# Kernel optimization log

Measured on AMD Instinct MI355X. Metric: run time of the kernel, lower is better.

Reference implementation:

```python
import jax, jax.numpy as jnp
import numpy as np
from jax import lax

B, T, V = 32, 2048, 32  # batch, num observations (frames), state vocabulary


def setup_inputs() -> dict:
    key = jax.random.key(0)
    k1, k2, k3, k4, k5 = jax.random.split(key, 5)
    inputs = jax.random.normal(k1, (B, T, V, V), dtype=jnp.float32)
    targets = jax.random.randint(k2, (B, T + 1), 0, V)  # state sequence z_0..z_T
    transition = 0.1 * jax.random.normal(k3, (V, V), dtype=jnp.float32)
    initial = 0.1 * jax.random.normal(k4, (V,), dtype=jnp.float32)
    final = 0.1 * jax.random.normal(k5, (V,), dtype=jnp.float32)
    return {"inputs": inputs, "transition": transition, "initial": initial,
            "final": final, "targets": targets}


def _log_prob(inputs, transition, initial, final, targets):
    # inputs: [B,T,V,V] arc scores score[b,t,i,j] for transition i->j at step t
    # Lattice semantics (compose(obs_fst, seq_fst)): a path is z_0..z_T with
    #   weight = initial[z_0] + sum_t (score[t, z_t, z_{t+1}] + A[z_t, z_{t+1}]) + final[z_T]
    b, t = inputs.shape[0], inputs.shape[1]
    v = transition.shape[0]

    # ---- denominator: forward algorithm (log-sum-exp DP over the lattice) ----
    scores_t = jnp.transpose(inputs, (1, 0, 2, 3))  # [T,B,V,V]
    alpha0 = jnp.broadcast_to(initial[None, :], (b, v))  # [B,V]

    def step(alpha, s_t):
        # alpha: [B,V] over previous state i; s_t: [B,V,V]
        m = alpha[:, :, None] + s_t + transition[None, :, :]  # [B,V,V]
        return jax.nn.logsumexp(m, axis=1), None

    alphaT, _ = lax.scan(step, alpha0, scores_t)
    denom = jax.nn.logsumexp(alphaT + final[None, :], axis=-1)  # [B]

    # ---- numerator: score of the ground-truth path ----
    y_prev = targets[:, :-1]  # [B,T]
    y_next = targets[:, 1:]   # [B,T]
    flat = inputs.reshape(b, t, v * v)
    emit = jnp.take_along_axis(flat, (y_prev * v + y_next)[..., None], axis=2)[..., 0]  # [B,T]
    trans = transition[y_prev, y_next]  # [B,T]
    num = (initial[targets[:, 0]]
           + jnp.sum(emit + trans, axis=1)
           + final[targets[:, -1]])  # [B]

    return num - denom  # log p(targets | inputs), per sequence: [B]


def reference(inputs, transition, initial, final, targets):
    return _log_prob(inputs, transition, initial, final, targets)
```

## Files before the change

### kernel.cpp

```cpp
#include <hip/hip_runtime.h>
#include <hip/hip_bf16.h>
#include <cmath>

#define Bz 32
#define Tz 2048
#define Vz 32
#define Cz 64
#define Lz 32
#define WPB 4

typedef short short8 __attribute__((ext_vector_type(8)));
typedef float f32x16 __attribute__((ext_vector_type(16)));
typedef float f32x4  __attribute__((ext_vector_type(4)));

static __device__ __forceinline__ unsigned short f2bf(float x) {
    unsigned u = __builtin_bit_cast(unsigned, x);
    u += 0x7FFFu + ((u >> 16) & 1u);
    return (unsigned short)(u >> 16);
}

static __device__ __forceinline__ void gl_lds16(const float* g, float* l) {
    __builtin_amdgcn_global_load_lds(
        (const __attribute__((address_space(1))) void*)g,
        (__attribute__((address_space(3))) void*)l, 16, 0, 0);
}

__global__ void __launch_bounds__(256) crf_chunks(
    const float* __restrict__ inputs, const float* __restrict__ trans,
    const int* __restrict__ targets, float* __restrict__ Pout,
    float* __restrict__ numpart)
{
    __shared__ __align__(16) float trans_lds[1024];
    __shared__ __align__(16) float sbuf[WPB][3 * 1024];
    __shared__ __align__(16) unsigned short elds[WPB][32 * 40];
    __shared__ __align__(16) float cbuf[WPB][32];

    const int tid  = threadIdx.x;
    const int lane = tid & 63;
    const int wid  = tid >> 6;
    const int gid  = __builtin_amdgcn_readfirstlane(blockIdx.x * WPB + wid);
    const int b    = gid >> 6;
    const int c    = gid & (Cz - 1);

    const int h = lane >> 5;
    const int j = lane & 31;
    const int kbase = 8 * h;

    float tr[16];
#pragma unroll
    for (int e = 0; e < 8; ++e) {
        tr[e]     = trans[(kbase + e) * Vz + j];
        tr[8 + e] = trans[(16 + kbase + e) * Vz + j];
    }

    ((float4*)trans_lds)[tid] = ((const float4*)trans)[tid];
    __syncthreads();

    const float* src = inputs + ((size_t)b * Tz + (size_t)c * Lz) * (Vz * Vz);
    const int*   tgb = targets + b * (Tz + 1) + c * Lz;
    int tgv = (lane < Lz + 1) ? tgb[lane] : 0;

    float* sw = sbuf[wid];
    {
        const float* g0 = src + lane * 4;
#pragma unroll
        for (int q = 0; q < 4; ++q) gl_lds16(g0 + q * 256, sw + q * 256);
        const float* g1 = src + 1024 + lane * 4;
#pragma unroll
        for (int q = 0; q < 4; ++q) gl_lds16(g1 + q * 256, sw + 1024 + q * 256);
    }

    f32x16 p;
    float cj = 0.f;
    float epart = 0.f;
    float ckr[16];
#pragma unroll
    for (int e = 0; e < 16; ++e) ckr[e] = 0.f;

    for (int t = 0; t < Lz; ++t) {
        if (t + 2 < Lz) {
            const float* g = src + (t + 2) * 1024 + lane * 4;
            float* dst = sw + ((t + 2) % 3) * 1024;
#pragma unroll
            for (int q = 0; q < 4; ++q) gl_lds16(g + q * 256, dst + q * 256);
        }
        const int rem = Lz - 1 - t;
        if (rem >= 2)      { asm volatile("s_waitcnt vmcnt(8)" ::: "memory"); }
        else if (rem == 1) { asm volatile("s_waitcnt vmcnt(4)" ::: "memory"); }
        else               { asm volatile("s_waitcnt vmcnt(0)" ::: "memory"); }
        __builtin_amdgcn_sched_barrier(0);

        const float* sb = sw + (t % 3) * 1024;

        {
            int yp = __shfl(tgv, t, 64);
            int yn = __shfl(tgv, t + 1, 64);
            int eidx = yp * Vz + yn;
            epart += sb[eidx] + trans_lds[eidx];
        }

        float m[16];
#pragma unroll
        for (int e = 0; e < 8; ++e) {
            m[e]     = sb[(kbase + e) * Vz + j]      + tr[e]     + ckr[e];
            m[8 + e] = sb[(16 + kbase + e) * Vz + j] + tr[8 + e] + ckr[8 + e];
        }
        float d = m[0];
#pragma unroll
        for (int e = 1; e < 16; ++e) d = fmaxf(d, m[e]);
        d = fmaxf(d, __shfl_xor(d, 32, 64));

        short8 B1, B2;
#pragma unroll
        for (int e = 0; e < 8; ++e) {
            B1[e] = (short)f2bf(__expf(m[e] - d));
            B2[e] = (short)f2bf(__expf(m[8 + e] - d));
        }

        short8 A1, A2;
        if (t == 0) {
#pragma unroll
            for (int e = 0; e < 8; ++e) {
                A1[e] = (short)((kbase + e == j) ? 0x3F80 : 0);
                A2[e] = (short)((16 + kbase + e == j) ? 0x3F80 : 0);
            }
        } else {
            const unsigned short* ew = elds[wid] + j * 40;
            A1 = *(const short8*)(ew + kbase);
            A2 = *(const short8*)(ew + 16 + kbase);
        }

        f32x16 z = {};
        p = __builtin_amdgcn_mfma_f32_32x32x16_bf16(A1, B1, z, 0, 0, 0);
        p = __builtin_amdgcn_mfma_f32_32x32x16_bf16(A2, B2, p, 0, 0, 0);

        float mj = p[0];
#pragma unroll
        for (int r = 1; r < 16; ++r) mj = fmaxf(mj, p[r]);
        mj = fmaxf(mj, __shfl_xor(mj, 32, 64));
        float inv = 1.0f / mj;
#pragma unroll
        for (int r = 0; r < 16; ++r) p[r] *= inv;
        cj = d + __logf(mj);

        unsigned short* ew = elds[wid];
#pragma unroll
        for (int r = 0; r < 16; ++r) {
            const int row = (r & 3) + 8 * (r >> 2) + 4 * h;
            ew[row * 40 + j] = f2bf(p[r]);
        }
        if (lane < 32) cbuf[wid][j] = cj;
        {
            const float* cb = cbuf[wid];
            f32x4 c0 = *(const f32x4*)(cb + kbase);
            f32x4 c1 = *(const f32x4*)(cb + kbase + 4);
            f32x4 c2 = *(const f32x4*)(cb + 16 + kbase);
            f32x4 c3 = *(const f32x4*)(cb + 16 + kbase + 4);
#pragma unroll
            for (int v = 0; v < 4; ++v) {
                ckr[v] = c0[v]; ckr[4 + v] = c1[v];
                ckr[8 + v] = c2[v]; ckr[12 + v] = c3[v];
            }
        }
    }

    float* Pc = Pout + (size_t)gid * 1024;
#pragma unroll
    for (int r = 0; r < 16; ++r) {
        const int row = (r & 3) + 8 * (r >> 2) + 4 * h;
        Pc[row * Vz + j] = cj + __logf(p[r]);
    }
    if (lane == 0) numpart[gid] = epart;
}

#define LOADQ(buf, chunk)                                                  \
    do { if ((chunk) < Cz) {                                               \
        const float* Pn = Pb + (size_t)(chunk) * 1024;                     \
        _Pragma("unroll")                                                  \
        for (int ii = 0; ii < 16; ++ii) buf[ii] = Pn[(hh + ii) * 32 + j];  \
    } } while (0)

#define PROCQ(buf)                                                         \
    do {                                                                   \
        float x[16];                                                       \
        _Pragma("unroll")                                                  \
        for (int ii = 0; ii < 16; ++ii)                                    \
            x[ii] = __shfl(al, hh + ii, 64) + buf[ii];                     \
        float u0 = fmaxf(x[0], x[1]),  u1 = fmaxf(x[2], x[3]);             \
        float u2 = fmaxf(x[4], x[5]),  u3 = fmaxf(x[6], x[7]);             \
        float u4 = fmaxf(x[8], x[9]),  u5 = fmaxf(x[10], x[11]);           \
        float u6 = fmaxf(x[12], x[13]), u7 = fmaxf(x[14], x[15]);          \
        u0 = fmaxf(u0, u1); u2 = fmaxf(u2, u3);                            \
        u4 = fmaxf(u4, u5); u6 = fmaxf(u6, u7);                            \
        u0 = fmaxf(u0, u2); u4 = fmaxf(u4, u6);                            \
        float mx = fmaxf(u0, u4);                                          \
        mx = fmaxf(mx, __shfl_xor(mx, 32, 64));                            \
        float e[16];                                                       \
        _Pragma("unroll")                                                  \
        for (int ii = 0; ii < 16; ++ii) e[ii] = __expf(x[ii] - mx);        \
        float s0 = e[0] + e[1],   s1 = e[2] + e[3];                        \
        float s2 = e[4] + e[5],   s3 = e[6] + e[7];                        \
        float s4 = e[8] + e[9],   s5 = e[10] + e[11];                      \
        float s6 = e[12] + e[13], s7 = e[14] + e[15];                      \
        s0 += s1; s2 += s3; s4 += s5; s6 += s7;                            \
        s0 += s2; s4 += s6;                                                \
        float s = s0 + s4;                                                 \
        s += __shfl_xor(s, 32, 64);                                        \
        al = mx + __logf(s);                                               \
    } while (0)

__global__ void __launch_bounds__(64) crf_combine(
    const float* __restrict__ Pout, const float* __restrict__ numpart,
    const float* __restrict__ initial, const float* __restrict__ fin,
    const int* __restrict__ targets, float* __restrict__ out)
{
    const int lane = threadIdx.x;
    const int b = blockIdx.x;
    const int h = lane >> 5;
    const int j = lane & 31;
    const int hh = h * 16;

    const float* Pb = Pout + (size_t)b * Cz * 1024;
    float al = initial[j];

    float q0[16], q1[16], q2[16], q3[16];
    LOADQ(q0, 0); LOADQ(q1, 1); LOADQ(q2, 2); LOADQ(q3, 3);

    for (int cc = 0; cc < Cz; cc += 4) {
        PROCQ(q0); LOADQ(q0, cc + 4);
        PROCQ(q1); LOADQ(q1, cc + 5);
        PROCQ(q2); LOADQ(q2, cc + 6);
        PROCQ(q3); LOADQ(q3, cc + 7);
    }

    float mm = (h == 0) ? (al + fin[j]) : -INFINITY;
    float ss = 1.f;
#pragma unroll
    for (int off = 32; off >= 1; off >>= 1) {
        float om = __shfl_xor(mm, off, 64);
        float os = __shfl_xor(ss, off, 64);
        float nm = fmaxf(mm, om);
        ss = ss * __expf(mm - nm) + os * __expf(om - nm);
        mm = nm;
    }
    float denom = mm + __logf(ss);

    float np = numpart[b * Cz + lane];
#pragma unroll
    for (int off = 32; off >= 1; off >>= 1) np += __shfl_xor(np, off, 64);

    if (lane == 0) {
        const int* tg = targets + b * (Tz + 1);
        out[b] = np + initial[tg[0]] + fin[tg[Tz]] - denom;
    }
}

extern "C" void kernel_launch(void* const* d_in, const int* in_sizes, int n_in,
                              void* d_out, int out_size, void* d_ws, size_t ws_size,
                              hipStream_t stream) {
    const float* inputs  = (const float*)d_in[0];
    const float* trans   = (const float*)d_in[1];
    const float* initial = (const float*)d_in[2];
    const float* fin     = (const float*)d_in[3];
    const int*   targets = (const int*)d_in[4];

    float* Pout    = (float*)d_ws;
    float* numpart = Pout + (size_t)Bz * Cz * 1024;

    hipLaunchKernelGGL(crf_chunks, dim3(Bz * Cz / WPB), dim3(256), 0, stream,
                       inputs, trans, targets, Pout, numpart);
    hipLaunchKernelGGL(crf_combine, dim3(Bz), dim3(64), 0, stream,
                       Pout, numpart, initial, fin, targets, (float*)d_out);
}
```

Measured before the change: 406.0 us.

## Fuse chunk and combine kernels via last-block atomic counter; deepen prefetch to 4 stages

```diff
diff --git a/kernel.cpp b/kernel.cpp
--- a/kernel.cpp
+++ b/kernel.cpp
@@ -8,6 +8,7 @@
 #define Cz 64
 #define Lz 32
 #define WPB 4
+#define BLK_PER_BATCH (Cz / WPB)
 
 typedef short short8 __attribute__((ext_vector_type(8)));
 typedef float f32x16 __attribute__((ext_vector_type(16)));
@@ -23,154 +24,6 @@
     __builtin_amdgcn_global_load_lds(
         (const __attribute__((address_space(1))) void*)g,
         (__attribute__((address_space(3))) void*)l, 16, 0, 0);
-}
-
-__global__ void __launch_bounds__(256) crf_chunks(
-    const float* __restrict__ inputs, const float* __restrict__ trans,
-    const int* __restrict__ targets, float* __restrict__ Pout,
-    float* __restrict__ numpart)
-{
-    __shared__ __align__(16) float trans_lds[1024];
-    __shared__ __align__(16) float sbuf[WPB][3 * 1024];
-    __shared__ __align__(16) unsigned short elds[WPB][32 * 40];
-    __shared__ __align__(16) float cbuf[WPB][32];
-
-    const int tid  = threadIdx.x;
-    const int lane = tid & 63;
-    const int wid  = tid >> 6;
-    const int gid  = __builtin_amdgcn_readfirstlane(blockIdx.x * WPB + wid);
-    const int b    = gid >> 6;
-    const int c    = gid & (Cz - 1);
-
-    const int h = lane >> 5;
-    const int j = lane & 31;
-    const int kbase = 8 * h;
-
-    float tr[16];
-#pragma unroll
-    for (int e = 0; e < 8; ++e) {
-        tr[e]     = trans[(kbase + e) * Vz + j];
-        tr[8 + e] = trans[(16 + kbase + e) * Vz + j];
-    }
-
-    ((float4*)trans_lds)[tid] = ((const float4*)trans)[tid];
-    __syncthreads();
-
-    const float* src = inputs + ((size_t)b * Tz + (size_t)c * Lz) * (Vz * Vz);
-    const int*   tgb = targets + b * (Tz + 1) + c * Lz;
-    int tgv = (lane < Lz + 1) ? tgb[lane] : 0;
-
-    float* sw = sbuf[wid];
-    {
-        const float* g0 = src + lane * 4;
-#pragma unroll
-        for (int q = 0; q < 4; ++q) gl_lds16(g0 + q * 256, sw + q * 256);
-        const float* g1 = src + 1024 + lane * 4;
-#pragma unroll
-        for (int q = 0; q < 4; ++q) gl_lds16(g1 + q * 256, sw + 1024 + q * 256);
-    }
-
-    f32x16 p;
-    float cj = 0.f;
-    float epart = 0.f;
-    float ckr[16];
-#pragma unroll
-    for (int e = 0; e < 16; ++e) ckr[e] = 0.f;
-
-    for (int t = 0; t < Lz; ++t) {
-        if (t + 2 < Lz) {
-            const float* g = src + (t + 2) * 1024 + lane * 4;
-            float* dst = sw + ((t + 2) % 3) * 1024;
-#pragma unroll
-            for (int q = 0; q < 4; ++q) gl_lds16(g + q * 256, dst + q * 256);
-        }
-        const int rem = Lz - 1 - t;
-        if (rem >= 2)      { asm volatile("s_waitcnt vmcnt(8)" ::: "memory"); }
-        else if (rem == 1) { asm volatile("s_waitcnt vmcnt(4)" ::: "memory"); }
-        else               { asm volatile("s_waitcnt vmcnt(0)" ::: "memory"); }
-        __builtin_amdgcn_sched_barrier(0);
-
-        const float* sb = sw + (t % 3) * 1024;
-
-        {
-            int yp = __shfl(tgv, t, 64);
-            int yn = __shfl(tgv, t + 1, 64);
-            int eidx = yp * Vz + yn;
-            epart += sb[eidx] + trans_lds[eidx];
-        }
-
-        float m[16];
-#pragma unroll
-        for (int e = 0; e < 8; ++e) {
-            m[e]     = sb[(kbase + e) * Vz + j]      + tr[e]     + ckr[e];
-            m[8 + e] = sb[(16 + kbase + e) * Vz + j] + tr[8 + e] + ckr[8 + e];
-        }
-        float d = m[0];
-#pragma unroll
-        for (int e = 1; e < 16; ++e) d = fmaxf(d, m[e]);
-        d = fmaxf(d, __shfl_xor(d, 32, 64));
-
-        short8 B1, B2;
-#pragma unroll
-        for (int e = 0; e < 8; ++e) {
-            B1[e] = (short)f2bf(__expf(m[e] - d));
-            B2[e] = (short)f2bf(__expf(m[8 + e] - d));
-        }
-
-        short8 A1, A2;
-        if (t == 0) {
-#pragma unroll
-            for (int e = 0; e < 8; ++e) {
-                A1[e] = (short)((kbase + e == j) ? 0x3F80 : 0);
-                A2[e] = (short)((16 + kbase + e == j) ? 0x3F80 : 0);
-            }
-        } else {
-            const unsigned short* ew = elds[wid] + j * 40;
-            A1 = *(const short8*)(ew + kbase);
-            A2 = *(const short8*)(ew + 16 + kbase);
-        }
-
-        f32x16 z = {};
-        p = __builtin_amdgcn_mfma_f32_32x32x16_bf16(A1, B1, z, 0, 0, 0);
-        p = __builtin_amdgcn_mfma_f32_32x32x16_bf16(A2, B2, p, 0, 0, 0);
-
-        float mj = p[0];
-#pragma unroll
-        for (int r = 1; r < 16; ++r) mj = fmaxf(mj, p[r]);
-        mj = fmaxf(mj, __shfl_xor(mj, 32, 64));
-        float inv = 1.0f / mj;
-#pragma unroll
-        for (int r = 0; r < 16; ++r) p[r] *= inv;
-        cj = d + __logf(mj);
-
-        unsigned short* ew = elds[wid];
-#pragma unroll
-        for (int r = 0; r < 16; ++r) {
-            const int row = (r & 3) + 8 * (r >> 2) + 4 * h;
-            ew[row * 40 + j] = f2bf(p[r]);
-        }
-        if (lane < 32) cbuf[wid][j] = cj;
-        {
-            const float* cb = cbuf[wid];
-            f32x4 c0 = *(const f32x4*)(cb + kbase);
-            f32x4 c1 = *(const f32x4*)(cb + kbase + 4);
-            f32x4 c2 = *(const f32x4*)(cb + 16 + kbase);
-            f32x4 c3 = *(const f32x4*)(cb + 16 + kbase + 4);
-#pragma unroll
-            for (int v = 0; v < 4; ++v) {
-                ckr[v] = c0[v]; ckr[4 + v] = c1[v];
-                ckr[8 + v] = c2[v]; ckr[12 + v] = c3[v];
-            }
-        }
-    }
-
-    float* Pc = Pout + (size_t)gid * 1024;
-#pragma unroll
-    for (int r = 0; r < 16; ++r) {
-        const int row = (r & 3) + 8 * (r >> 2) + 4 * h;
-        Pc[row * Vz + j] = cj + __logf(p[r]);
-    }
-    if (lane == 0) numpart[gid] = epart;
 }
 
 #define LOADQ(buf, chunk)                                                  \
@@ -209,23 +62,165 @@
         al = mx + __logf(s);                                               \
     } while (0)
 
-__global__ void __launch_bounds__(64) crf_combine(
-    const float* __restrict__ Pout, const float* __restrict__ numpart,
-    const float* __restrict__ initial, const float* __restrict__ fin,
-    const int* __restrict__ targets, float* __restrict__ out)
+__global__ void __launch_bounds__(256) crf_fused(
+    const float* __restrict__ inputs, const float* __restrict__ trans,
+    const int* __restrict__ targets, const float* __restrict__ initial,
+    const float* __restrict__ fin, float* __restrict__ Pout,
+    float* __restrict__ numpart, int* __restrict__ cnt, float* __restrict__ out)
 {
-    const int lane = threadIdx.x;
-    const int b = blockIdx.x;
+    __shared__ __align__(16) float trans_lds[1024];
+    __shared__ __align__(16) float sbuf[WPB][4 * 1024];
+    __shared__ __align__(16) unsigned short elds[WPB][32 * 40];
+    __shared__ __align__(16) float cbuf[WPB][32];
+    __shared__ int lastflag;
+
+    const int tid  = threadIdx.x;
+    const int lane = tid & 63;
+    const int wid  = tid >> 6;
+    const int gid  = __builtin_amdgcn_readfirstlane(blockIdx.x * WPB + wid);
+    const int b    = gid >> 6;
+    const int c    = gid & (Cz - 1);
+
     const int h = lane >> 5;
     const int j = lane & 31;
+    const int kbase = 8 * h;
+
+    float tr[16];
+#pragma unroll
+    for (int e = 0; e < 8; ++e) {
+        tr[e]     = trans[(kbase + e) * Vz + j];
+        tr[8 + e] = trans[(16 + kbase + e) * Vz + j];
+    }
+    ((float4*)trans_lds)[tid] = ((const float4*)trans)[tid];
+    __syncthreads();
+
+    const float* src = inputs + ((size_t)b * Tz + (size_t)c * Lz) * (Vz * Vz);
+    const int*   tgb = targets + b * (Tz + 1) + c * Lz;
+    int tgv = (lane < Lz + 1) ? tgb[lane] : 0;
+
+    float* sw = sbuf[wid];
+#pragma unroll
+    for (int pt = 0; pt < 3; ++pt) {
+        const float* g = src + pt * 1024 + lane * 4;
+#pragma unroll
+        for (int q = 0; q < 4; ++q) gl_lds16(g + q * 256, sw + pt * 1024 + q * 256);
+    }
+
+    f32x16 p;
+    float cj = 0.f, epart = 0.f;
+    float ckr[16];
+#pragma unroll
+    for (int e = 0; e < 16; ++e) ckr[e] = 0.f;
+
+    for (int t = 0; t < Lz; ++t) {
+        if (t + 3 < Lz) {
+            const float* g = src + (t + 3) * 1024 + lane * 4;
+            float* dst = sw + ((t + 3) & 3) * 1024;
+#pragma unroll
+            for (int q = 0; q < 4; ++q) gl_lds16(g + q * 256, dst + q * 256);
+        }
+        const int rem = Lz - 1 - t;
+        if (rem >= 3)      { asm volatile("s_waitcnt vmcnt(12)" ::: "memory"); }
+        else if (rem == 2) { asm volatile("s_waitcnt vmcnt(8)"  ::: "memory"); }
+        else if (rem == 1) { asm volatile("s_waitcnt vmcnt(4)"  ::: "memory"); }
+        else               { asm volatile("s_waitcnt vmcnt(0)"  ::: "memory"); }
+        __builtin_amdgcn_sched_barrier(0);
+
+        const float* sb = sw + (t & 3) * 1024;
+
+        {
+            int yp = __shfl(tgv, t, 64);
+            int yn = __shfl(tgv, t + 1, 64);
+            int eidx = yp * Vz + yn;
+            epart += sb[eidx] + trans_lds[eidx];
+        }
+
+        float m[16];
+#pragma unroll
+        for (int e = 0; e < 8; ++e) {
+            m[e]     = sb[(kbase + e) * Vz + j]      + tr[e]     + ckr[e];
+            m[8 + e] = sb[(16 + kbase + e) * Vz + j] + tr[8 + e] + ckr[8 + e];
+        }
+        float d = m[0];
+#pragma unroll
+        for (int e = 1; e < 16; ++e) d = fmaxf(d, m[e]);
+        d = fmaxf(d, __shfl_xor(d, 32, 64));
+
+        short8 B1, B2;
+#pragma unroll
+        for (int e = 0; e < 8; ++e) {
+            B1[e] = (short)f2bf(__expf(m[e] - d));
+            B2[e] = (short)f2bf(__expf(m[8 + e] - d));
+        }
+
+        short8 A1, A2;
+        if (t == 0) {
+#pragma unroll
+            for (int e = 0; e < 8; ++e) {
+                A1[e] = (short)((kbase + e == j) ? 0x3F80 : 0);
+                A2[e] = (short)((16 + kbase + e == j) ? 0x3F80 : 0);
+            }
+        } else {
+            const unsigned short* ew = elds[wid] + j * 40;
+            A1 = *(const short8*)(ew + kbase);
+            A2 = *(const short8*)(ew + 16 + kbase);
+        }
+
+        f32x16 z = {};
+        p = __builtin_amdgcn_mfma_f32_32x32x16_bf16(A1, B1, z, 0, 0, 0);
+        p = __builtin_amdgcn_mfma_f32_32x32x16_bf16(A2, B2, p, 0, 0, 0);
+
+        float mj = p[0];
+#pragma unroll
+        for (int r = 1; r < 16; ++r) mj = fmaxf(mj, p[r]);
+        mj = fmaxf(mj, __shfl_xor(mj, 32, 64));
+        float inv = 1.0f / mj;
+#pragma unroll
+        for (int r = 0; r < 16; ++r) p[r] *= inv;
+        cj = d + __logf(mj);
+
+        unsigned short* ew = elds[wid];
+#pragma unroll
+        for (int r = 0; r < 16; ++r) {
+            const int row = (r & 3) + 8 * (r >> 2) + 4 * h;
+            ew[row * 40 + j] = f2bf(p[r]);
+        }
+        if (lane < 32) cbuf[wid][j] = cj;
+        {
+            const float* cb = cbuf[wid];
+            f32x4 c0 = *(const f32x4*)(cb + kbase);
+            f32x4 c1 = *(const f32x4*)(cb + kbase + 4);
+            f32x4 c2 = *(const f32x4*)(cb + 16 + kbase);
+            f32x4 c3 = *(const f32x4*)(cb + 16 + kbase + 4);
+#pragma unroll
+            for (int v = 0; v < 4; ++v) {
+                ckr[v] = c0[v]; ckr[4 + v] = c1[v];
+                ckr[8 + v] = c2[v]; ckr[12 + v] = c3[v];
+            }
+        }
+    }
+
+    float* Pc = Pout + (size_t)gid * 1024;
+#pragma unroll
+    for (int r = 0; r < 16; ++r) {
+        const int row = (r & 3) + 8 * (r >> 2) + 4 * h;
+        Pc[row * Vz + j] = cj + __logf(p[r]);
+    }
+    if (lane == 0) numpart[gid] = epart;
+
+    __threadfence();
+    __syncthreads();
+    if (tid == 0) lastflag = (atomicAdd(&cnt[b], 1) == BLK_PER_BATCH - 1);
+    __syncthreads();
+    if (!lastflag || tid >= 64) return;
+    __threadfence();
+
     const int hh = h * 16;
-
     const float* Pb = Pout + (size_t)b * Cz * 1024;
     float al = initial[j];
 
     float q0[16], q1[16], q2[16], q3[16];
     LOADQ(q0, 0); LOADQ(q1, 1); LOADQ(q2, 2); LOADQ(q3, 3);
-
     for (int cc = 0; cc < Cz; cc += 4) {
         PROCQ(q0); LOADQ(q0, cc + 4);
         PROCQ(q1); LOADQ(q1, cc + 5);
@@ -266,9 +261,10 @@
 
     float* Pout    = (float*)d_ws;
     float* numpart = Pout + (size_t)Bz * Cz * 1024;
-
-    hipLaunchKernelGGL(crf_chunks, dim3(Bz * Cz / WPB), dim3(256), 0, stream,
-                       inputs, trans, targets, Pout, numpart);
-    hipLaunchKernelGGL(crf_combine, dim3(Bz), dim3(64), 0, stream,
-                       Pout, numpart, initial, fin, targets, (float*)d_out);
-}
+    int*   cnt     = (int*)(numpart + Bz * Cz);
+
+    hipMemsetAsync(cnt, 0, Bz * sizeof(int), stream);
+    hipLaunchKernelGGL(crf_fused, dim3(Bz * Cz / WPB), dim3(256), 0, stream,
+                       inputs, trans, targets, initial, fin,
+                       Pout, numpart, cnt, (float*)d_out);
+}
```

New measurement: 486.6 us. 1.2x slower.
